# Kernel tuning notes

Hardware: AMD Instinct MI355X
Metric: run time of the kernel (lower is better)

The kernel has to match this reference:

```python
import jax, jax.numpy as jnp
import numpy as np

BETA = 0.25
K, D = 1024, 64


def setup_inputs() -> dict:
    key = jax.random.key(0)
    k1, k2 = jax.random.split(key)
    z = jax.random.normal(k1, (2, D, 32, 32, 32), dtype=jnp.float32)
    # nn.Embedding initialized uniform(-1/K, 1/K)
    embedding = jax.random.uniform(k2, (K, D), dtype=jnp.float32,
                                   minval=-1.0 / K, maxval=1.0 / K)
    return {"z": z, "embedding": embedding}


def reference(z, embedding):
    # z: [B, D, X, Y, Z] -> [B, X, Y, Z, D]
    zp = jnp.transpose(z, (0, 2, 3, 4, 1))
    latents_shape = zp.shape
    flat = zp.reshape(-1, embedding.shape[1])  # [N, D]

    dist = (jnp.sum(flat ** 2, axis=1, keepdims=True)
            + jnp.sum(embedding ** 2, axis=1)
            - 2.0 * flat @ embedding.T)
    min_encoding_indices = jnp.argmin(dist, axis=1)  # [N]

    z_q = embedding[min_encoding_indices].reshape(latents_shape)

    commitment_loss = jnp.mean((jax.lax.stop_gradient(z_q) - zp) ** 2)
    embedding_loss = jnp.mean((z_q - jax.lax.stop_gradient(zp)) ** 2)
    vq_loss = commitment_loss * BETA + embedding_loss  # point=False branch

    # straight-through estimator
    z_q_st = zp + jax.lax.stop_gradient(z_q - zp)
    out = jnp.transpose(z_q_st, (0, 4, 1, 2, 3))  # back to [B, D, X, Y, Z]
    return out, vq_loss, min_encoding_indices[:, None]
```

## Files before the change

### kernel.cpp

```cpp
#include <hip/hip_runtime.h>
#include <hip/hip_fp16.h>

#define KDIM 1024
#define DDIM 64
#define SPAT 32768
#define NVEC 65536
#define DSP  (DDIM * SPAT)
#define MARGIN 5.0e-4f
#define ZPAD 65
#define QCAP 1536

typedef _Float16 half8 __attribute__((ext_vector_type(8)));
typedef float floatx4 __attribute__((ext_vector_type(4)));

__device__ __forceinline__ float opaque(float x) { asm volatile("" : "+v"(x)); return x; }

__device__ __forceinline__ unsigned int f2s(float x) {
    unsigned int u = __float_as_uint(x);
    return u ^ ((u >> 31) ? 0xffffffffu : 0x80000000u);
}
__device__ __forceinline__ float s2f(unsigned int u) {
    unsigned int v = u ^ ((u & 0x80000000u) ? 0x80000000u : 0xffffffffu);
    return __uint_as_float(v);
}

__device__ __forceinline__ float np_sumsq64(const float* x) {
    float r8[8];
#pragma unroll
    for (int j = 0; j < 8; ++j) r8[j] = opaque(x[1 + j] * x[1 + j]);
#pragma unroll
    for (int i = 8; i < 56; i += 8) {
#pragma unroll
        for (int j = 0; j < 8; ++j) r8[j] += opaque(x[1 + i + j] * x[1 + i + j]);
    }
    float res = ((r8[0] + r8[1]) + (r8[2] + r8[3])) + ((r8[4] + r8[5]) + (r8[6] + r8[7]));
#pragma unroll
    for (int m = 57; m < 64; ++m) res += opaque(x[m] * x[m]);
    return opaque(x[0] * x[0]) + res;
}

__device__ __forceinline__ unsigned long long exact_score(
    const float* zr, float snr, const float* __restrict__ e2_,
    const float* __restrict__ h_, int k)
{
    const float* ep = e2_ + (size_t)k * DDIM;
    float acc = 0.f;
#pragma unroll
    for (int d = 0; d < DDIM; ++d)
        acc = fmaf(ep[d], zr[d], acc);
    float tt   = snr + h_[k];
    float dist = tt - acc;
    return ((unsigned long long)__float_as_uint(dist) << 32) | (unsigned int)k;
}

__global__ void vq_prep_e(const float* __restrict__ emb, float* __restrict__ e2,
                          float* __restrict__ h, __half* __restrict__ eh) {
    __shared__ float L[64 * ZPAD];
    const int tid = threadIdx.x;
    const int kbase = blockIdx.x * 64;
    const float* src = emb + (size_t)kbase * DDIM;
#pragma unroll
    for (int i = 0; i < 16; ++i) {
        int g = i * 256 + tid;
        L[(g >> 6) * ZPAD + (g & 63)] = src[g];
    }
    __syncthreads();
#pragma unroll
    for (int i = 0; i < 16; ++i) {
        int g = i * 256 + tid;
        float v = L[(g >> 6) * ZPAD + (g & 63)];
        e2[(size_t)kbase * DDIM + g] = v + v;
        eh[(size_t)kbase * DDIM + g] = (__half)(_Float16)(v * 1024.0f);
    }
    if (tid < 64) h[kbase + tid] = np_sumsq64(&L[tid * ZPAD]);
}

__global__ __launch_bounds__(256, 4) void vq_mfma_kernel(
    const float* __restrict__ z, const float* __restrict__ emb,
    const __half* __restrict__ eh_, const float* __restrict__ h_,
    const float* __restrict__ e2_, float* __restrict__ out,
    float* __restrict__ loss, float* __restrict__ idxf)
{
    __shared__ float zrow[64 * ZPAD];
    __shared__ float lds_sn[64];
    __shared__ unsigned int m1bits[64];
    __shared__ int qcnt;
    __shared__ unsigned short     qk[QCAP];
    __shared__ unsigned char      qn[QCAP];
    __shared__ unsigned long long rbest[64];

    const int tid = threadIdx.x, l = tid & 63, w = tid >> 6;
    const int nbase = blockIdx.x * 64;
    const int b = nbase >> 15, s0 = nbase & (SPAT - 1);
    const int col16 = l & 15, g16 = l >> 4;
    const float* zbase = z + (size_t)b * DSP + s0;

    if (tid == 0) qcnt = 0;
    if (tid < 64) { rbest[tid] = ~0ull; m1bits[tid] = 0xffffffffu; }

    {
        const int dbase = w * 16;
#pragma unroll
        for (int j = 0; j < 16; ++j)
            zrow[l * ZPAD + dbase + j] = zbase[(size_t)(dbase + j) * SPAT + l];
    }
    __syncthreads();

    if (tid < 64) lds_sn[tid] = np_sumsq64(&zrow[tid * ZPAD]);

    half8 zf[4][2];
#pragma unroll
    for (int nc = 0; nc < 4; ++nc) {
        const int r = nc * 16 + col16;
#pragma unroll
        for (int kp = 0; kp < 2; ++kp) {
            const int d0 = g16 * 8 + kp * 32;
            half8 vh;
#pragma unroll
            for (int u = 0; u < 8; ++u)
                vh[u] = (_Float16)zrow[r * ZPAD + d0 + u];
            zf[nc][kp] = vh;
        }
    }

    const int myk0 = w * 256;
    half8 f0[3], f1[3]; floatx4 fh[3];
#define LOADT(slot, t) { \
        const size_t o_ = (size_t)(myk0 + (t) * 16 + col16) * DDIM + g16 * 8; \
        f0[slot] = *(const half8*)(eh_ + o_); \
        f1[slot] = *(const half8*)(eh_ + o_ + 32); \
        fh[slot] = *(const floatx4*)(h_ + myk0 + (t) * 16 + g16 * 4); }

    float m1[4];
#pragma unroll
    for (int nc = 0; nc < 4; ++nc) m1[nc] = 3.0e38f;
    LOADT(0, 0) LOADT(1, 1)
#pragma unroll
    for (int t = 0; t < 16; ++t) {
        const int cs = t % 3;
        if (t < 14) LOADT((t + 2) % 3, t + 2)
#pragma unroll
        for (int nc = 0; nc < 4; ++nc) {
            floatx4 acc = {0.f, 0.f, 0.f, 0.f};
            acc = __builtin_amdgcn_mfma_f32_16x16x32_f16(f0[cs], zf[nc][0], acc, 0, 0, 0);
            acc = __builtin_amdgcn_mfma_f32_16x16x32_f16(f1[cs], zf[nc][1], acc, 0, 0, 0);
#pragma unroll
            for (int j = 0; j < 4; ++j)
                m1[nc] = fminf(m1[nc], fmaf(-0.001953125f, acc[j], fh[cs][j]));
        }
    }
#pragma unroll
    for (int nc = 0; nc < 4; ++nc)
        atomicMin(&m1bits[nc * 16 + col16], f2s(m1[nc]));
    __syncthreads();

    float thr[4];
#pragma unroll
    for (int nc = 0; nc < 4; ++nc) thr[nc] = s2f(m1bits[nc * 16 + col16]) + MARGIN;

    LOADT(0, 0) LOADT(1, 1)
#pragma unroll
    for (int t = 0; t < 16; ++t) {
        const int cs = t % 3;
        if (t < 14) LOADT((t + 2) % 3, t + 2)
        const int rbase = myk0 + t * 16 + g16 * 4;
#pragma unroll
        for (int nc = 0; nc < 4; ++nc) {
            floatx4 acc = {0.f, 0.f, 0.f, 0.f};
            acc = __builtin_amdgcn_mfma_f32_16x16x32_f16(f0[cs], zf[nc][0], acc, 0, 0, 0);
            acc = __builtin_amdgcn_mfma_f32_16x16x32_f16(f1[cs], zf[nc][1], acc, 0, 0, 0);
#pragma unroll
            for (int j = 0; j < 4; ++j) {
                float dist = fmaf(-0.001953125f, acc[j], fh[cs][j]);
                if (dist <= thr[nc]) {
                    int p = atomicAdd(&qcnt, 1);
                    if (p < QCAP) {
                        qk[p] = (unsigned short)(rbase + j);
                        qn[p] = (unsigned char)(nc * 16 + col16);
                    }
                }
            }
        }
    }
#undef LOADT
    __syncthreads();

    const int qlen = min(qcnt, QCAP);
    for (int i = tid; i < qlen; i += 256) {
        const int r = qn[i];
        atomicMin(&rbest[r], exact_score(&zrow[r * ZPAD], lds_sn[r], e2_, h_, qk[i]));
    }
    __syncthreads();

    if (qcnt > QCAP) {
        const int row = tid & 63, kq = tid >> 6;
        for (int k = kq * 256; k < kq * 256 + 256; ++k)
            atomicMin(&rbest[row], exact_score(&zrow[row * ZPAD], lds_sn[row], e2_, h_, k));
        __syncthreads();
    }

    if (tid < 64) {
        const int I1 = (int)(rbest[tid] & 0xffffffffu);
        const int n = nbase + tid;
        idxf[n] = (float)I1;

        const float* e = emb + (size_t)I1 * DDIM;
        float* op = out + (size_t)b * DSP + s0 + tid;
        float lsum = 0.f;
#pragma unroll
        for (int d = 0; d < DDIM; ++d) {
            float qv = e[d];
            op[(size_t)d * SPAT] = qv;
            float df = qv - zrow[tid * ZPAD + d];
            lsum = fmaf(df, df, lsum);
        }
#pragma unroll
        for (int off = 32; off > 0; off >>= 1)
            lsum += __shfl_down(lsum, off, 64);
        if (tid == 0)
            atomicAdd(loss, lsum * (1.25f / 4194304.0f));
    }
}

extern "C" void kernel_launch(void* const* d_in, const int* in_sizes, int n_in,
                              void* d_out, int out_size, void* d_ws, size_t ws_size,
                              hipStream_t stream) {
    const float* z   = (const float*)d_in[0];
    const float* emb = (const float*)d_in[1];
    float* out  = (float*)d_out;
    float* loss = out + 4194304;
    float* idxf = out + 4194305;

    float* h_  = (float*)d_ws;
    float* e2_ = h_ + KDIM;
    __half* eh_ = (__half*)(e2_ + KDIM * DDIM);

    hipMemsetAsync(loss, 0, sizeof(float), stream);
    vq_prep_e<<<KDIM / 64, 256, 0, stream>>>(emb, e2_, h_, eh_);
    vq_mfma_kernel<<<NVEC / 64, 256, 0, stream>>>(z, emb, eh_, h_, e2_, out, loss, idxf);
}
```

Before: 71.56 us.

## Stage codebook tiles into LDS via direct global-to-LDS loads, cache norms, parallelize epilogue

Replaces the register-prefetched global loads of fp16 codebook fragments with double-buffered global_load_lds staging into swizzled per-wave LDS buffers, and caches the codebook norms in LDS. It also drops the precomputed 2*e buffer in favour of scaling on the fly, adds a wave-level __any early-out around candidate enqueueing, and tightens MARGIN, QCAP and ZPAD. The epilogue now spreads the output write and loss computation across all four waves instead of one. The tighter margin and smaller queue raise the risk of overflow into the slow exhaustive fallback or of missing the true argmin.

```diff
diff --git a/kernel.cpp b/kernel.cpp
--- a/kernel.cpp
+++ b/kernel.cpp
@@ -6,9 +6,9 @@
 #define SPAT 32768
 #define NVEC 65536
 #define DSP  (DDIM * SPAT)
-#define MARGIN 5.0e-4f
-#define ZPAD 65
-#define QCAP 1536
+#define MARGIN 3.0e-4f
+#define ZPAD 68
+#define QCAP 384
 
 typedef _Float16 half8 __attribute__((ext_vector_type(8)));
 typedef float floatx4 __attribute__((ext_vector_type(4)));
@@ -40,21 +40,21 @@
 }
 
 __device__ __forceinline__ unsigned long long exact_score(
-    const float* zr, float snr, const float* __restrict__ e2_,
-    const float* __restrict__ h_, int k)
+    const float* zr, float snr, const float* __restrict__ emb,
+    const float* h_lds, int k)
 {
-    const float* ep = e2_ + (size_t)k * DDIM;
+    const float* ep = emb + (size_t)k * DDIM;
     float acc = 0.f;
 #pragma unroll
     for (int d = 0; d < DDIM; ++d)
-        acc = fmaf(ep[d], zr[d], acc);
-    float tt   = snr + h_[k];
+        acc = fmaf(2.0f * ep[d], zr[d], acc);
+    float tt   = snr + h_lds[k];
     float dist = tt - acc;
     return ((unsigned long long)__float_as_uint(dist) << 32) | (unsigned int)k;
 }
 
-__global__ void vq_prep_e(const float* __restrict__ emb, float* __restrict__ e2,
-                          float* __restrict__ h, __half* __restrict__ eh) {
+__global__ void vq_prep_e(const float* __restrict__ emb, float* __restrict__ h,
+                          __half* __restrict__ eh) {
     __shared__ float L[64 * ZPAD];
     const int tid = threadIdx.x;
     const int kbase = blockIdx.x * 64;
@@ -68,26 +68,27 @@
 #pragma unroll
     for (int i = 0; i < 16; ++i) {
         int g = i * 256 + tid;
-        float v = L[(g >> 6) * ZPAD + (g & 63)];
-        e2[(size_t)kbase * DDIM + g] = v + v;
-        eh[(size_t)kbase * DDIM + g] = (__half)(_Float16)(v * 1024.0f);
+        eh[(size_t)kbase * DDIM + g] = (__half)(_Float16)(L[(g >> 6) * ZPAD + (g & 63)] * 1024.0f);
     }
     if (tid < 64) h[kbase + tid] = np_sumsq64(&L[tid * ZPAD]);
 }
 
-__global__ __launch_bounds__(256, 4) void vq_mfma_kernel(
+extern "C" __global__
+__attribute__((amdgpu_flat_work_group_size(256, 256), amdgpu_waves_per_eu(4, 4)))
+void vq_mfma_kernel(
     const float* __restrict__ z, const float* __restrict__ emb,
     const __half* __restrict__ eh_, const float* __restrict__ h_,
-    const float* __restrict__ e2_, float* __restrict__ out,
-    float* __restrict__ loss, float* __restrict__ idxf)
+    float* __restrict__ out, float* __restrict__ loss, float* __restrict__ idxf)
 {
     __shared__ float zrow[64 * ZPAD];
+    __shared__ float h_lds[KDIM];
     __shared__ float lds_sn[64];
     __shared__ unsigned int m1bits[64];
     __shared__ int qcnt;
-    __shared__ unsigned short     qk[QCAP];
-    __shared__ unsigned char      qn[QCAP];
+    __shared__ unsigned short qk[QCAP];
+    __shared__ unsigned char  qn[QCAP];
     __shared__ unsigned long long rbest[64];
+    __shared__ __align__(16) char ebuf[4][2][2048];
 
     const int tid = threadIdx.x, l = tid & 63, w = tid >> 6;
     const int nbase = blockIdx.x * 64;
@@ -98,6 +99,7 @@
     if (tid == 0) qcnt = 0;
     if (tid < 64) { rbest[tid] = ~0ull; m1bits[tid] = 0xffffffffu; }
 
+    ((float4*)h_lds)[tid] = ((const float4*)h_)[tid];
     {
         const int dbase = w * 16;
 #pragma unroll
@@ -124,29 +126,42 @@
     }
 
     const int myk0 = w * 256;
-    half8 f0[3], f1[3]; floatx4 fh[3];
-#define LOADT(slot, t) { \
-        const size_t o_ = (size_t)(myk0 + (t) * 16 + col16) * DDIM + g16 * 8; \
-        f0[slot] = *(const half8*)(eh_ + o_); \
-        f1[slot] = *(const half8*)(eh_ + o_ + 32); \
-        fh[slot] = *(const floatx4*)(h_ + myk0 + (t) * 16 + g16 * 4); }
+    const int swl  = ((l >> 3) & 7) << 4;
+    const int src0 = (l * 16) ^ swl;
+    const int src1 = 1024 + ((l * 16) ^ swl);
+    const int rd0 = (col16 * 128 + g16 * 16) ^ ((col16 & 7) << 4);
+
+#define STAGE(t, buf) { \
+        const char* gsrc = (const char*)(eh_ + (size_t)(myk0 + (t) * 16) * DDIM); \
+        char* db = &ebuf[w][buf][0]; \
+        __builtin_amdgcn_global_load_lds((const __attribute__((address_space(1))) void*)(gsrc + src0), \
+                                         (__attribute__((address_space(3))) void*)db, 16, 0, 0); \
+        __builtin_amdgcn_global_load_lds((const __attribute__((address_space(1))) void*)(gsrc + src1), \
+                                         (__attribute__((address_space(3))) void*)(db + 1024), 16, 0, 0); }
 
     float m1[4];
 #pragma unroll
     for (int nc = 0; nc < 4; ++nc) m1[nc] = 3.0e38f;
-    LOADT(0, 0) LOADT(1, 1)
+    STAGE(0, 0) STAGE(1, 1)
 #pragma unroll
     for (int t = 0; t < 16; ++t) {
-        const int cs = t % 3;
-        if (t < 14) LOADT((t + 2) % 3, t + 2)
+        const int buf = t & 1;
+        if (t < 15) asm volatile("s_waitcnt vmcnt(2)" ::: "memory");
+        else        asm volatile("s_waitcnt vmcnt(0)" ::: "memory");
+        const char* tb = &ebuf[w][buf][0];
+        half8 f0 = *(const half8*)(tb + rd0);
+        half8 f1 = *(const half8*)(tb + (rd0 ^ 64));
+        floatx4 hv = *(const floatx4*)(&h_lds[myk0 + t * 16 + g16 * 4]);
+        asm volatile("" :: "v"((floatx4)f0), "v"((floatx4)f1));
+        if (t < 14) STAGE(t + 2, buf)
 #pragma unroll
         for (int nc = 0; nc < 4; ++nc) {
             floatx4 acc = {0.f, 0.f, 0.f, 0.f};
-            acc = __builtin_amdgcn_mfma_f32_16x16x32_f16(f0[cs], zf[nc][0], acc, 0, 0, 0);
-            acc = __builtin_amdgcn_mfma_f32_16x16x32_f16(f1[cs], zf[nc][1], acc, 0, 0, 0);
+            acc = __builtin_amdgcn_mfma_f32_16x16x32_f16(f0, zf[nc][0], acc, 0, 0, 0);
+            acc = __builtin_amdgcn_mfma_f32_16x16x32_f16(f1, zf[nc][1], acc, 0, 0, 0);
 #pragma unroll
             for (int j = 0; j < 4; ++j)
-                m1[nc] = fminf(m1[nc], fmaf(-0.001953125f, acc[j], fh[cs][j]));
+                m1[nc] = fminf(m1[nc], fmaf(-0.001953125f, acc[j], hv[j]));
         }
     }
 #pragma unroll
@@ -158,66 +173,78 @@
 #pragma unroll
     for (int nc = 0; nc < 4; ++nc) thr[nc] = s2f(m1bits[nc * 16 + col16]) + MARGIN;
 
-    LOADT(0, 0) LOADT(1, 1)
+    STAGE(0, 0) STAGE(1, 1)
 #pragma unroll
     for (int t = 0; t < 16; ++t) {
-        const int cs = t % 3;
-        if (t < 14) LOADT((t + 2) % 3, t + 2)
+        const int buf = t & 1;
+        if (t < 15) asm volatile("s_waitcnt vmcnt(2)" ::: "memory");
+        else        asm volatile("s_waitcnt vmcnt(0)" ::: "memory");
+        const char* tb = &ebuf[w][buf][0];
+        half8 f0 = *(const half8*)(tb + rd0);
+        half8 f1 = *(const half8*)(tb + (rd0 ^ 64));
+        floatx4 hv = *(const floatx4*)(&h_lds[myk0 + t * 16 + g16 * 4]);
+        asm volatile("" :: "v"((floatx4)f0), "v"((floatx4)f1));
+        if (t < 14) STAGE(t + 2, buf)
         const int rbase = myk0 + t * 16 + g16 * 4;
 #pragma unroll
         for (int nc = 0; nc < 4; ++nc) {
             floatx4 acc = {0.f, 0.f, 0.f, 0.f};
-            acc = __builtin_amdgcn_mfma_f32_16x16x32_f16(f0[cs], zf[nc][0], acc, 0, 0, 0);
-            acc = __builtin_amdgcn_mfma_f32_16x16x32_f16(f1[cs], zf[nc][1], acc, 0, 0, 0);
-#pragma unroll
-            for (int j = 0; j < 4; ++j) {
-                float dist = fmaf(-0.001953125f, acc[j], fh[cs][j]);
-                if (dist <= thr[nc]) {
-                    int p = atomicAdd(&qcnt, 1);
-                    if (p < QCAP) {
-                        qk[p] = (unsigned short)(rbase + j);
-                        qn[p] = (unsigned char)(nc * 16 + col16);
+            acc = __builtin_amdgcn_mfma_f32_16x16x32_f16(f0, zf[nc][0], acc, 0, 0, 0);
+            acc = __builtin_amdgcn_mfma_f32_16x16x32_f16(f1, zf[nc][1], acc, 0, 0, 0);
+            float d0 = fmaf(-0.001953125f, acc[0], hv[0]);
+            float d1 = fmaf(-0.001953125f, acc[1], hv[1]);
+            float d2 = fmaf(-0.001953125f, acc[2], hv[2]);
+            float d3 = fmaf(-0.001953125f, acc[3], hv[3]);
+            if (__any((d0 <= thr[nc]) | (d1 <= thr[nc]) | (d2 <= thr[nc]) | (d3 <= thr[nc]))) {
+#pragma unroll
+                for (int j = 0; j < 4; ++j) {
+                    float dj = (j == 0) ? d0 : (j == 1) ? d1 : (j == 2) ? d2 : d3;
+                    if (dj <= thr[nc]) {
+                        int p = atomicAdd(&qcnt, 1);
+                        if (p < QCAP) {
+                            qk[p] = (unsigned short)(rbase + j);
+                            qn[p] = (unsigned char)(nc * 16 + col16);
+                        }
                     }
                 }
             }
         }
     }
-#undef LOADT
+#undef STAGE
     __syncthreads();
 
     const int qlen = min(qcnt, QCAP);
     for (int i = tid; i < qlen; i += 256) {
         const int r = qn[i];
-        atomicMin(&rbest[r], exact_score(&zrow[r * ZPAD], lds_sn[r], e2_, h_, qk[i]));
+        atomicMin(&rbest[r], exact_score(&zrow[r * ZPAD], lds_sn[r], emb, h_lds, qk[i]));
     }
     __syncthreads();
 
     if (qcnt > QCAP) {
         const int row = tid & 63, kq = tid >> 6;
         for (int k = kq * 256; k < kq * 256 + 256; ++k)
-            atomicMin(&rbest[row], exact_score(&zrow[row * ZPAD], lds_sn[row], e2_, h_, k));
+            atomicMin(&rbest[row], exact_score(&zrow[row * ZPAD], lds_sn[row], emb, h_lds, k));
         __syncthreads();
     }
 
-    if (tid < 64) {
-        const int I1 = (int)(rbest[tid] & 0xffffffffu);
-        const int n = nbase + tid;
-        idxf[n] = (float)I1;
-
-        const float* e = emb + (size_t)I1 * DDIM;
-        float* op = out + (size_t)b * DSP + s0 + tid;
+    if (tid < 64) idxf[nbase + tid] = (float)(unsigned int)(rbest[tid] & 0xffffffffu);
+    {
+        const int I1 = (int)(rbest[l] & 0xffffffffu);
+        const int dbase = w * 16;
+        float* opb = out + (size_t)b * DSP + s0;
         float lsum = 0.f;
 #pragma unroll
-        for (int d = 0; d < DDIM; ++d) {
-            float qv = e[d];
-            op[(size_t)d * SPAT] = qv;
-            float df = qv - zrow[tid * ZPAD + d];
+        for (int j = 0; j < 16; ++j) {
+            const int d = dbase + j;
+            float qv = emb[(size_t)I1 * DDIM + d];
+            opb[(size_t)d * SPAT + l] = qv;
+            float df = qv - zrow[l * ZPAD + d];
             lsum = fmaf(df, df, lsum);
         }
 #pragma unroll
         for (int off = 32; off > 0; off >>= 1)
             lsum += __shfl_down(lsum, off, 64);
-        if (tid == 0)
+        if (l == 0)
             atomicAdd(loss, lsum * (1.25f / 4194304.0f));
     }
 }
@@ -232,10 +259,10 @@
     float* idxf = out + 4194305;
 
     float* h_  = (float*)d_ws;
-    float* e2_ = h_ + KDIM;
-    __half* eh_ = (__half*)(e2_ + KDIM * DDIM);
+    __half* eh_ = (__half*)(h_ + KDIM);
 
     hipMemsetAsync(loss, 0, sizeof(float), stream);
-    vq_prep_e<<<KDIM / 64, 256, 0, stream>>>(emb, e2_, h_, eh_);
-    vq_mfma_kernel<<<NVEC / 64, 256, 0, stream>>>(z, emb, eh_, h_, e2_, out, loss, idxf);
-}
+    vq_prep_e<<<KDIM / 64, 256, 0, stream>>>(emb, h_, eh_);
+    hipLaunchKernelGGL(vq_mfma_kernel, dim3(NVEC / 64), dim3(256), 0, stream,
+                       z, emb, eh_, h_, out, loss, idxf);
+}
```

Measured after the change: 91.99 us. +28.5%, slower.

## Fold codebook norms into MFMA accumulator init and spread epilogue across all waves

Applied to the files above, without the earlier changes.

Precomputes -512*||e||^2 and passes it as the MFMA accumulator input, so the per-element scaling fma turns into a max reduction over the raw scores. The threshold now works in scaled-accumulator units with a matching margin, and the candidate queue capacity shrinks. The epilogue gather/store and the loss sum are split across all four waves instead of one, and the z-norm computation is spread too. The memset is folded into the prep kernel, and the e2 buffer is dropped in favour of reading emb and doubling inline. Risks include a changed margin equivalence and more full-scan fallbacks if the smaller queue overflows.

```diff
diff --git a/kernel.cpp b/kernel.cpp
--- a/kernel.cpp
+++ b/kernel.cpp
@@ -6,9 +6,9 @@
 #define SPAT 32768
 #define NVEC 65536
 #define DSP  (DDIM * SPAT)
-#define MARGIN 5.0e-4f
+#define MARGIN_ACC 0.25f
 #define ZPAD 65
-#define QCAP 1536
+#define QCAP 512
 
 typedef _Float16 half8 __attribute__((ext_vector_type(8)));
 typedef float floatx4 __attribute__((ext_vector_type(4)));
@@ -40,53 +40,50 @@
 }
 
 __device__ __forceinline__ unsigned long long exact_score(
-    const float* zr, float snr, const float* __restrict__ e2_,
+    const float* zr, float snr, const float* __restrict__ emb,
     const float* __restrict__ h_, int k)
 {
-    const float* ep = e2_ + (size_t)k * DDIM;
+    const float* ep = emb + (size_t)k * DDIM;
     float acc = 0.f;
 #pragma unroll
     for (int d = 0; d < DDIM; ++d)
-        acc = fmaf(ep[d], zr[d], acc);
+        acc = fmaf(2.0f * ep[d], zr[d], acc);
     float tt   = snr + h_[k];
     float dist = tt - acc;
     return ((unsigned long long)__float_as_uint(dist) << 32) | (unsigned int)k;
 }
 
-__global__ void vq_prep_e(const float* __restrict__ emb, float* __restrict__ e2,
-                          float* __restrict__ h, __half* __restrict__ eh) {
-    __shared__ float L[64 * ZPAD];
+__global__ void vq_prep_e(const float* __restrict__ emb, float* __restrict__ h,
+                          float* __restrict__ hneg, __half* __restrict__ eh,
+                          float* __restrict__ loss) {
     const int tid = threadIdx.x;
-    const int kbase = blockIdx.x * 64;
-    const float* src = emb + (size_t)kbase * DDIM;
-#pragma unroll
-    for (int i = 0; i < 16; ++i) {
+    const int kbase = blockIdx.x * 16;
+#pragma unroll
+    for (int i = 0; i < 4; ++i) {
         int g = i * 256 + tid;
-        L[(g >> 6) * ZPAD + (g & 63)] = src[g];
-    }
-    __syncthreads();
-#pragma unroll
-    for (int i = 0; i < 16; ++i) {
-        int g = i * 256 + tid;
-        float v = L[(g >> 6) * ZPAD + (g & 63)];
-        e2[(size_t)kbase * DDIM + g] = v + v;
+        float v = emb[(size_t)kbase * DDIM + g];
         eh[(size_t)kbase * DDIM + g] = (__half)(_Float16)(v * 1024.0f);
     }
-    if (tid < 64) h[kbase + tid] = np_sumsq64(&L[tid * ZPAD]);
+    if (tid < 16) {
+        float s = np_sumsq64(emb + (size_t)(kbase + tid) * DDIM);
+        h[kbase + tid]    = s;
+        hneg[kbase + tid] = -512.0f * s;
+    }
+    if (blockIdx.x == 0 && tid == 0) *loss = 0.f;
 }
 
 __global__ __launch_bounds__(256, 4) void vq_mfma_kernel(
     const float* __restrict__ z, const float* __restrict__ emb,
     const __half* __restrict__ eh_, const float* __restrict__ h_,
-    const float* __restrict__ e2_, float* __restrict__ out,
+    const float* __restrict__ hneg_, float* __restrict__ out,
     float* __restrict__ loss, float* __restrict__ idxf)
 {
     __shared__ float zrow[64 * ZPAD];
     __shared__ float lds_sn[64];
     __shared__ unsigned int m1bits[64];
     __shared__ int qcnt;
-    __shared__ unsigned short     qk[QCAP];
-    __shared__ unsigned char      qn[QCAP];
+    __shared__ unsigned short qk[QCAP];
+    __shared__ unsigned char  qn[QCAP];
     __shared__ unsigned long long rbest[64];
 
     const int tid = threadIdx.x, l = tid & 63, w = tid >> 6;
@@ -96,7 +93,7 @@
     const float* zbase = z + (size_t)b * DSP + s0;
 
     if (tid == 0) qcnt = 0;
-    if (tid < 64) { rbest[tid] = ~0ull; m1bits[tid] = 0xffffffffu; }
+    if (tid < 64) { rbest[tid] = ~0ull; m1bits[tid] = 0u; }
 
     {
         const int dbase = w * 16;
@@ -106,7 +103,7 @@
     }
     __syncthreads();
 
-    if (tid < 64) lds_sn[tid] = np_sumsq64(&zrow[tid * ZPAD]);
+    if (l < 16) lds_sn[w * 16 + l] = np_sumsq64(&zrow[(w * 16 + l) * ZPAD]);
 
     half8 zf[4][2];
 #pragma unroll
@@ -124,16 +121,16 @@
     }
 
     const int myk0 = w * 256;
-    half8 f0[3], f1[3]; floatx4 fh[3];
+    half8 f0[3], f1[3]; floatx4 hc[3];
 #define LOADT(slot, t) { \
         const size_t o_ = (size_t)(myk0 + (t) * 16 + col16) * DDIM + g16 * 8; \
         f0[slot] = *(const half8*)(eh_ + o_); \
         f1[slot] = *(const half8*)(eh_ + o_ + 32); \
-        fh[slot] = *(const floatx4*)(h_ + myk0 + (t) * 16 + g16 * 4); }
+        hc[slot] = *(const floatx4*)(hneg_ + myk0 + (t) * 16 + g16 * 4); }
 
     float m1[4];
 #pragma unroll
-    for (int nc = 0; nc < 4; ++nc) m1[nc] = 3.0e38f;
+    for (int nc = 0; nc < 4; ++nc) m1[nc] = -3.0e38f;
     LOADT(0, 0) LOADT(1, 1)
 #pragma unroll
     for (int t = 0; t < 16; ++t) {
@@ -141,22 +138,19 @@
         if (t < 14) LOADT((t + 2) % 3, t + 2)
 #pragma unroll
         for (int nc = 0; nc < 4; ++nc) {
-            floatx4 acc = {0.f, 0.f, 0.f, 0.f};
-            acc = __builtin_amdgcn_mfma_f32_16x16x32_f16(f0[cs], zf[nc][0], acc, 0, 0, 0);
+            floatx4 acc = __builtin_amdgcn_mfma_f32_16x16x32_f16(f0[cs], zf[nc][0], hc[cs], 0, 0, 0);
             acc = __builtin_amdgcn_mfma_f32_16x16x32_f16(f1[cs], zf[nc][1], acc, 0, 0, 0);
-#pragma unroll
-            for (int j = 0; j < 4; ++j)
-                m1[nc] = fminf(m1[nc], fmaf(-0.001953125f, acc[j], fh[cs][j]));
+            m1[nc] = fmaxf(m1[nc], fmaxf(fmaxf(acc[0], acc[1]), fmaxf(acc[2], acc[3])));
         }
     }
 #pragma unroll
     for (int nc = 0; nc < 4; ++nc)
-        atomicMin(&m1bits[nc * 16 + col16], f2s(m1[nc]));
+        atomicMax(&m1bits[nc * 16 + col16], f2s(m1[nc]));
     __syncthreads();
 
     float thr[4];
 #pragma unroll
-    for (int nc = 0; nc < 4; ++nc) thr[nc] = s2f(m1bits[nc * 16 + col16]) + MARGIN;
+    for (int nc = 0; nc < 4; ++nc) thr[nc] = s2f(m1bits[nc * 16 + col16]) - MARGIN_ACC;
 
     LOADT(0, 0) LOADT(1, 1)
 #pragma unroll
@@ -166,13 +160,11 @@
         const int rbase = myk0 + t * 16 + g16 * 4;
 #pragma unroll
         for (int nc = 0; nc < 4; ++nc) {
-            floatx4 acc = {0.f, 0.f, 0.f, 0.f};
-            acc = __builtin_amdgcn_mfma_f32_16x16x32_f16(f0[cs], zf[nc][0], acc, 0, 0, 0);
+            floatx4 acc = __builtin_amdgcn_mfma_f32_16x16x32_f16(f0[cs], zf[nc][0], hc[cs], 0, 0, 0);
             acc = __builtin_amdgcn_mfma_f32_16x16x32_f16(f1[cs], zf[nc][1], acc, 0, 0, 0);
 #pragma unroll
             for (int j = 0; j < 4; ++j) {
-                float dist = fmaf(-0.001953125f, acc[j], fh[cs][j]);
-                if (dist <= thr[nc]) {
+                if (acc[j] >= thr[nc]) {
                     int p = atomicAdd(&qcnt, 1);
                     if (p < QCAP) {
                         qk[p] = (unsigned short)(rbase + j);
@@ -188,36 +180,35 @@
     const int qlen = min(qcnt, QCAP);
     for (int i = tid; i < qlen; i += 256) {
         const int r = qn[i];
-        atomicMin(&rbest[r], exact_score(&zrow[r * ZPAD], lds_sn[r], e2_, h_, qk[i]));
+        atomicMin(&rbest[r], exact_score(&zrow[r * ZPAD], lds_sn[r], emb, h_, qk[i]));
     }
     __syncthreads();
 
     if (qcnt > QCAP) {
         const int row = tid & 63, kq = tid >> 6;
         for (int k = kq * 256; k < kq * 256 + 256; ++k)
-            atomicMin(&rbest[row], exact_score(&zrow[row * ZPAD], lds_sn[row], e2_, h_, k));
+            atomicMin(&rbest[row], exact_score(&zrow[row * ZPAD], lds_sn[row], emb, h_, k));
         __syncthreads();
     }
 
-    if (tid < 64) {
-        const int I1 = (int)(rbest[tid] & 0xffffffffu);
-        const int n = nbase + tid;
-        idxf[n] = (float)I1;
-
-        const float* e = emb + (size_t)I1 * DDIM;
-        float* op = out + (size_t)b * DSP + s0 + tid;
+    if (tid < 64) idxf[nbase + tid] = (float)(unsigned int)(rbest[tid] & 0xffffffffu);
+    {
+        const int I1 = (int)(rbest[l] & 0xffffffffu);
+        const int dbase = w * 16;
+        float* opb = out + (size_t)b * DSP + s0;
         float lsum = 0.f;
 #pragma unroll
-        for (int d = 0; d < DDIM; ++d) {
-            float qv = e[d];
-            op[(size_t)d * SPAT] = qv;
-            float df = qv - zrow[tid * ZPAD + d];
+        for (int j = 0; j < 16; ++j) {
+            const int d = dbase + j;
+            float qv = emb[(size_t)I1 * DDIM + d];
+            opb[(size_t)d * SPAT + l] = qv;
+            float df = qv - zrow[l * ZPAD + d];
             lsum = fmaf(df, df, lsum);
         }
 #pragma unroll
         for (int off = 32; off > 0; off >>= 1)
             lsum += __shfl_down(lsum, off, 64);
-        if (tid == 0)
+        if (l == 0)
             atomicAdd(loss, lsum * (1.25f / 4194304.0f));
     }
 }
@@ -231,11 +222,10 @@
     float* loss = out + 4194304;
     float* idxf = out + 4194305;
 
-    float* h_  = (float*)d_ws;
-    float* e2_ = h_ + KDIM;
-    __half* eh_ = (__half*)(e2_ + KDIM * DDIM);
-
-    hipMemsetAsync(loss, 0, sizeof(float), stream);
-    vq_prep_e<<<KDIM / 64, 256, 0, stream>>>(emb, e2_, h_, eh_);
-    vq_mfma_kernel<<<NVEC / 64, 256, 0, stream>>>(z, emb, eh_, h_, e2_, out, loss, idxf);
-}
+    float* h_    = (float*)d_ws;
+    float* hneg_ = h_ + KDIM;
+    __half* eh_  = (__half*)(hneg_ + KDIM);
+
+    vq_prep_e<<<KDIM / 16, 256, 0, stream>>>(emb, h_, hneg_, eh_, loss);
+    vq_mfma_kernel<<<NVEC / 64, 256, 0, stream>>>(z, emb, eh_, h_, hneg_, out, loss, idxf);
+}
```

Measured after the change: 103.6 us. +44.7%, slower.
